# Optimization experiments

Hardware: AMD Instinct MI355X
Metric: run time of the kernel (lower is better)

Reference implementation:

```python
import jax, jax.numpy as jnp
import numpy as np

N_HEAD = 16


def setup_inputs() -> dict:
    key = jax.random.key(0)
    ks = jax.random.split(key, 4)
    B, S, NX = 2, 2048, 1024
    x = jax.random.normal(ks[0], (B, S, NX), dtype=jnp.float32)
    # additive causal mask: 0 where j <= i, -1e9 where j > i
    causal = jnp.tril(jnp.ones((S, S), dtype=jnp.float32))
    attention_mask = ((1.0 - causal) * -1e9)[None, None, :, :]
    w_attn = jax.random.normal(ks[1], (NX, 3 * NX), dtype=jnp.float32) * 0.02
    b_attn = jnp.zeros((3 * NX,), dtype=jnp.float32)
    w_proj = jax.random.normal(ks[2], (NX, NX), dtype=jnp.float32) * 0.02
    b_proj = jnp.zeros((NX,), dtype=jnp.float32)
    return {"x": x, "attention_mask": attention_mask, "w_attn": w_attn,
            "b_attn": b_attn, "w_proj": w_proj, "b_proj": b_proj}


def reference(x, attention_mask, w_attn, b_attn, w_proj, b_proj):
    B, S, NX = x.shape
    H = N_HEAD
    D = NX // H
    # c_attn (Conv1D): x @ W + b -> [B, S, 3*NX]
    qkv = jnp.einsum('bse,ef->bsf', x, w_attn) + b_attn
    q, k, v = jnp.split(qkv, 3, axis=-1)
    # split heads -> [B, H, S, D]
    q = q.reshape(B, S, H, D).transpose(0, 2, 1, 3)
    k = k.reshape(B, S, H, D).transpose(0, 2, 1, 3)
    v = v.reshape(B, S, H, D).transpose(0, 2, 1, 3)
    # scores [B, H, S, S], scaled by 1/sqrt(head_dim) since scale=True
    w = jnp.einsum('bhqd,bhkd->bhqk', q, k) / jnp.sqrt(jnp.float32(D))
    w = w + attention_mask
    w = jax.nn.softmax(w, axis=-1)
    # attn_dropout is identity in eval / p=0
    a = jnp.einsum('bhqk,bhkd->bhqd', w, v)
    # merge heads -> [B, S, NX]
    a = a.transpose(0, 2, 1, 3).reshape(B, S, NX)
    # c_proj (Conv1D)
    out = jnp.einsum('bse,ef->bsf', a, w_proj) + b_proj
    # resid_dropout identity
    return out
```

## Files before the change

### kernel.cpp

```cpp
#include <hip/hip_runtime.h>
#include <hip/hip_bf16.h>

typedef __bf16 bf16;
typedef __bf16 bf16x8 __attribute__((ext_vector_type(8)));
typedef __bf16 bf16x4 __attribute__((ext_vector_type(4)));
typedef float  f32x4  __attribute__((ext_vector_type(4)));
typedef float  f32x16 __attribute__((ext_vector_type(16)));

#define MFMA16(A,B,C) __builtin_amdgcn_mfma_f32_16x16x32_bf16(A,B,C,0,0,0)
#define MFMA32(A,B,C) __builtin_amdgcn_mfma_f32_32x32x16_bf16(A,B,C,0,0,0)
#define EXP2(x) __builtin_amdgcn_exp2f(x)

static constexpr int SEQ = 2048;
static constexpr int NXC = 1024;
#define QSCALE 0.1803368801111244f

static __device__ inline unsigned packb(float lo, float hi) {
  union { bf16 h[2]; unsigned u; } x;
  x.h[0] = (bf16)lo; x.h[1] = (bf16)hi;
  return x.u;
}
static __device__ inline bf16x8 frag_from_words(unsigned a, unsigned b,
                                                unsigned c, unsigned d) {
  union { unsigned u[4]; bf16x8 v; } x;
  x.u[0] = a; x.u[1] = b; x.u[2] = c; x.u[3] = d;
  return x.v;
}
__device__ __forceinline__ void gload16(const bf16* g, bf16* l) {
  __builtin_amdgcn_global_load_lds(
      (const __attribute__((address_space(1))) void*)g,
      (__attribute__((address_space(3))) void*)l, 16, 0, 0);
}

__global__ __launch_bounds__(256) void f2b_kernel(const float* __restrict__ in,
                                                  bf16* __restrict__ out, int n4) {
  int i = blockIdx.x * blockDim.x + threadIdx.x;
  if (i < n4) {
    float4 v = ((const float4*)in)[i];
    bf16x4 o;
    o[0] = (bf16)v.x; o[1] = (bf16)v.y; o[2] = (bf16)v.z; o[3] = (bf16)v.w;
    ((bf16x4*)out)[i] = o;
  }
}

__global__ __launch_bounds__(256) void tr_f2b(const float* __restrict__ in,
                                              bf16* __restrict__ out, int R, int C) {
  __shared__ bf16 t[64][72];
  const int c0 = blockIdx.x * 64, r0 = blockIdx.y * 64;
  const int tid = threadIdx.x;
  const int lr = tid >> 4, lc = (tid & 15) * 4;
  #pragma unroll
  for (int p = 0; p < 4; ++p) {
    int rr = lr + p * 16;
    float4 v = *(const float4*)&in[(size_t)(r0 + rr) * C + c0 + lc];
    t[lc + 0][rr] = (bf16)v.x; t[lc + 1][rr] = (bf16)v.y;
    t[lc + 2][rr] = (bf16)v.z; t[lc + 3][rr] = (bf16)v.w;
  }
  __syncthreads();
  const int orow = tid >> 3, ocol = (tid & 7) * 8;
  #pragma unroll
  for (int p = 0; p < 2; ++p) {
    int rr = orow + p * 32;
    *(bf16x8*)&out[(size_t)(c0 + rr) * R + r0 + ocol] = *(const bf16x8*)&t[rr][ocol];
  }
}

template<int MODE>
__global__ __launch_bounds__(256, 3) void gemm_bt(
    const bf16* __restrict__ A, const bf16* __restrict__ BT,
    const float* __restrict__ bias,
    bf16* __restrict__ qb, bf16* __restrict__ kb, bf16* __restrict__ vtb,
    float* __restrict__ outf, int K, int N, int nb)
{
  __shared__ bf16 As[2][128 * 32];
  __shared__ bf16 Bs[2][128 * 32];

  const int tid  = threadIdx.x;
  const int lane = tid & 63;
  const int w    = tid >> 6;
  const int cpx  = gridDim.x >> 3;
  const int swzb = (blockIdx.x & 7) * cpx + (blockIdx.x >> 3);
  const int m0   = (swzb / nb) * 128;
  const int n0   = (swzb % nb) * 128;
  const int wrow = (w >> 1) * 64;
  const int wcol = (w & 1) * 64;
  const int g    = lane >> 4;
  const int c16  = lane & 15;

  f32x4 acc[4][4];
  #pragma unroll
  for (int i = 0; i < 4; ++i)
    #pragma unroll
    for (int j = 0; j < 4; ++j)
      acc[i][j] = f32x4{0.f, 0.f, 0.f, 0.f};

  const int srow = lane >> 2;
  const int scol = ((lane & 3) ^ ((lane >> 3) & 3)) * 8;
  const bf16* gA = A  + (size_t)(m0 + w * 16 + srow) * K + scol;
  const bf16* gB = BT + (size_t)(n0 + w * 16 + srow) * K + scol;
  const size_t rstep = (size_t)64 * K;
  const int rchunk = (g ^ ((c16 >> 1) & 3)) * 8;

  const int NT = K >> 5;

  auto STAGE = [&](int b, int k0) {
    bf16* lA = &As[b][w * 512];
    bf16* lB = &Bs[b][w * 512];
    gload16(gA + k0,         lA);
    gload16(gA + k0 + rstep, lA + 64 * 32);
    gload16(gB + k0,         lB);
    gload16(gB + k0 + rstep, lB + 64 * 32);
  };

  STAGE(0, 0);
  __syncthreads();

  int cur = 0;
  for (int t = 0; t < NT; ++t) {
    if (t + 1 < NT) STAGE(cur ^ 1, (t + 1) << 5);

    const bf16* pa = &As[cur][0];
    const bf16* pb = &Bs[cur][0];
    bf16x8 af[4], bfr[4];
    #pragma unroll
    for (int i = 0; i < 4; ++i)
      af[i] = *(const bf16x8*)&pa[(wrow + i * 16 + c16) * 32 + rchunk];
    #pragma unroll
    for (int j = 0; j < 4; ++j)
      bfr[j] = *(const bf16x8*)&pb[(wcol + j * 16 + c16) * 32 + rchunk];
    #pragma unroll
    for (int i = 0; i < 4; ++i)
      #pragma unroll
      for (int j = 0; j < 4; ++j)
        acc[i][j] = MFMA16(af[i], bfr[j], acc[i][j]);

    __syncthreads();
    cur ^= 1;
  }

  #pragma unroll
  for (int i = 0; i < 4; ++i) {
    #pragma unroll
    for (int j = 0; j < 4; ++j) {
      #pragma unroll
      for (int r = 0; r < 4; ++r) {
        int gm = m0 + wrow + i * 16 + g * 4 + r;
        int gn = n0 + wcol + j * 16 + c16;
        float v = acc[i][j][r] + bias[gn];
        if (MODE == 0) {
          int which = gn >> 10;
          int cc = gn & 1023;
          int hh = cc >> 6, dd = cc & 63;
          int bb = gm >> 11, ss = gm & 2047;
          int bh = bb * 16 + hh;
          if (which == 0)
            qb[((size_t)bh * SEQ + ss) * 64 + dd] = (bf16)(v * QSCALE);
          else if (which == 1)
            kb[((size_t)bh * SEQ + ss) * 64 + dd] = (bf16)v;
          else
            vtb[((size_t)bh * 64 + dd) * SEQ + ss] = (bf16)v;
        } else {
          outf[(size_t)gm * N + gn] = v;
        }
      }
    }
  }
}

__global__ __launch_bounds__(256, 2) void attn9_kernel(
    const bf16* __restrict__ q, const bf16* __restrict__ k,
    const bf16* __restrict__ vt, bf16* __restrict__ aout)
{
  __shared__ bf16 smem[2][8192];

  const int tid  = threadIdx.x;
  const int lane = tid & 63;
  const int w    = tid >> 6;
  const int hi   = lane >> 5;
  const int q_l  = lane & 31;
  const int bid  = blockIdx.x;
  const int bh   = bid & 31;
  const int idx8 = (bid & 255) >> 5;
  const int strip= (bid >> 8) ? idx8 : 15 - idx8;
  const int qr0  = strip * 128 + w * 32;
  const int qg   = qr0 + q_l;
  const int nt   = 2 * strip + 2;

  bf16x8 qf[4];
  {
    const bf16* qp = q + ((size_t)bh * SEQ + qr0 + q_l) * 64 + hi * 8;
    #pragma unroll
    for (int c = 0; c < 4; ++c) qf[c] = *(const bf16x8*)(qp + c * 16);
  }

  f32x16 Ot0 = (f32x16)0.f, Ot1 = (f32x16)0.f;
  float mrun = -INFINITY, lrun = 0.f;

  const int r1 = tid >> 3;
  const int c1 = (tid & 7) ^ (r1 & 7);
  const bf16* kB = k  + (size_t)bh * SEQ * 64;
  const bf16* vB = vt + (size_t)bh * 64 * SEQ;
  const int sw = q_l & 7;

  auto STAGE = [&](int b, int kv0) {
    bf16* buf = &smem[b][0];
    gload16(kB + (size_t)(kv0 + r1) * 64 + c1 * 8,       buf + w * 512);
    gload16(kB + (size_t)(kv0 + r1 + 32) * 64 + c1 * 8,  buf + 2048 + w * 512);
    gload16(vB + (size_t)r1 * SEQ + kv0 + c1 * 8,        buf + 4096 + w * 512);
    gload16(vB + (size_t)(r1 + 32) * SEQ + kv0 + c1 * 8, buf + 6144 + w * 512);
  };

  auto do_tile = [&](int b, int kv0) {
    const bf16* Kb = &smem[b][0];
    const bf16* Vb = &smem[b][4096];

    bf16x8 kf[8];
    #pragma unroll
    for (int c = 0; c < 4; ++c) {
      int ch = ((2 * c + hi) ^ sw) * 8;
      kf[c]     = *(const bf16x8*)&Kb[q_l * 64 + ch];
      kf[4 + c] = *(const bf16x8*)&Kb[(q_l + 32) * 64 + ch];
    }

    f32x16 st0 = (f32x16)0.f, st1 = (f32x16)0.f;
    __builtin_amdgcn_s_setprio(1);
    #pragma unroll
    for (int c = 0; c < 4; ++c) {
      st0 = MFMA32(kf[c],     qf[c], st0);
      st1 = MFMA32(kf[4 + c], qf[c], st1);
    }
    __builtin_amdgcn_s_setprio(0);

    bf16x8 vf[8];
    #pragma unroll
    for (int t2 = 0; t2 < 2; ++t2)
      #pragma unroll
      for (int h = 0; h < 2; ++h) {
        int ch = ((4 * t2 + 2 * h + hi) ^ sw) * 8;
        vf[t2 * 2 + h]     = *(const bf16x8*)&Vb[q_l * 64 + ch];
        vf[4 + t2 * 2 + h] = *(const bf16x8*)&Vb[(q_l + 32) * 64 + ch];
      }

    if (kv0 + 63 > qr0) {
      #pragma unroll
      for (int r = 0; r < 16; ++r) {
        int kvl = kv0 + (r & 3) + 8 * (r >> 2) + 4 * hi;
        if (kvl > qg)      st0[r] = -1e30f;
        if (kvl + 32 > qg) st1[r] = -1e30f;
      }
    }

    float m8[8];
    #pragma unroll
    for (int r = 0; r < 8; ++r)
      m8[r] = fmaxf(fmaxf(st0[r], st0[r + 8]), fmaxf(st1[r], st1[r + 8]));
    #pragma unroll
    for (int r = 0; r < 4; ++r) m8[r] = fmaxf(m8[r], m8[r + 4]);
    float pmax = fmaxf(fmaxf(m8[0], m8[1]), fmaxf(m8[2], m8[3]));

    float mnew;
    if (__all(pmax <= mrun + 8.f)) {
      mnew = mrun;
    } else {
      float pm = fmaxf(pmax, __shfl_xor(pmax, 32));
      mnew = fmaxf(mrun, pm);
      const float sc = EXP2(mrun - mnew);
      lrun *= sc;
      Ot0 *= sc;
      Ot1 *= sc;
      mrun = mnew;
    }

    #pragma unroll
    for (int r = 0; r < 16; ++r) {
      st0[r] = EXP2(st0[r] - mnew);
      st1[r] = EXP2(st1[r] - mnew);
    }

    float s8[8];
    #pragma unroll
    for (int r = 0; r < 8; ++r)
      s8[r] = (st0[r] + st0[r + 8]) + (st1[r] + st1[r + 8]);
    #pragma unroll
    for (int r = 0; r < 4; ++r) s8[r] += s8[r + 4];
    lrun += (s8[0] + s8[1]) + (s8[2] + s8[3]);

    unsigned pw[16];
    #pragma unroll
    for (int m = 0; m < 8; ++m) {
      pw[m]     = packb(st0[2 * m], st0[2 * m + 1]);
      pw[8 + m] = packb(st1[2 * m], st1[2 * m + 1]);
    }
    __builtin_amdgcn_s_setprio(1);
    #pragma unroll
    for (int t2 = 0; t2 < 2; ++t2) {
      #pragma unroll
      for (int h = 0; h < 2; ++h) {
        auto sa = __builtin_amdgcn_permlane32_swap((int)pw[t2 * 8 + 4 * h + 0],
                                                   (int)pw[t2 * 8 + 4 * h + 2], false, false);
        auto sb = __builtin_amdgcn_permlane32_swap((int)pw[t2 * 8 + 4 * h + 1],
                                                   (int)pw[t2 * 8 + 4 * h + 3], false, false);
        bf16x8 pb = frag_from_words((unsigned)sa[0], (unsigned)sb[0],
                                    (unsigned)sa[1], (unsigned)sb[1]);
        Ot0 = MFMA32(vf[t2 * 2 + h],     pb, Ot0);
        Ot1 = MFMA32(vf[4 + t2 * 2 + h], pb, Ot1);
      }
    }
    __builtin_amdgcn_s_setprio(0);
  };

  STAGE(0, 0);
  asm volatile("s_waitcnt vmcnt(0)" ::: "memory");
  __builtin_amdgcn_s_barrier();

  int cur = 0;
  for (int t = 0; t < nt - 1; ++t) {
    STAGE(cur ^ 1, (t + 1) << 6);
    if ((t << 6) <= qr0 + 31) do_tile(cur, t << 6);
    asm volatile("s_waitcnt vmcnt(0)" ::: "memory");
    __builtin_amdgcn_s_barrier();
    cur ^= 1;
  }
  do_tile(cur, (nt - 1) << 6);

  lrun += __shfl_xor(lrun, 32);
  const float inv = 1.f / lrun;

  __syncthreads();
  bf16* ot = &smem[0][0];
  const int orow = w * 32 + q_l;
  #pragma unroll
  for (int r = 0; r < 16; ++r) {
    int d = (r & 3) + 8 * (r >> 2) + 4 * hi;
    ot[orow * 72 + d]      = (bf16)(Ot0[r] * inv);
    ot[orow * 72 + d + 32] = (bf16)(Ot1[r] * inv);
  }
  __syncthreads();

  const int bb = bh >> 4, hh = bh & 15;
  const int qrow = w * 32 + (lane >> 1), half = lane & 1;
  const bf16* src = ot + qrow * 72 + half * 32;
  bf16* dst = aout + ((size_t)bb * SEQ + strip * 128 + qrow) * NXC + hh * 64 + half * 32;
  #pragma unroll
  for (int e = 0; e < 4; ++e)
    *(bf16x8*)(dst + e * 8) = *(const bf16x8*)(src + e * 8);
}

extern "C" void kernel_launch(void* const* d_in, const int* in_sizes, int n_in,
                              void* d_out, int out_size, void* d_ws, size_t ws_size,
                              hipStream_t stream) {
  const float* x      = (const float*)d_in[0];
  const float* w_attn = (const float*)d_in[2];
  const float* b_attn = (const float*)d_in[3];
  const float* w_proj = (const float*)d_in[4];
  const float* b_proj = (const float*)d_in[5];
  float* out = (float*)d_out;

  char* p = (char*)d_ws;
  bf16* xb   = (bf16*)p; p += (size_t)4194304 * 2;
  bf16* wabT = (bf16*)p; p += (size_t)3145728 * 2;
  bf16* wpbT = (bf16*)p; p += (size_t)1048576 * 2;
  bf16* qb   = (bf16*)p; p += (size_t)4194304 * 2;
  bf16* kb   = (bf16*)p; p += (size_t)4194304 * 2;
  bf16* vtb  = (bf16*)p; p += (size_t)4194304 * 2;
  bf16* ab   = (bf16*)p; p += (size_t)4194304 * 2;

  f2b_kernel<<<4096, 256, 0, stream>>>(x, xb, 1048576);
  tr_f2b<<<dim3(48, 16), 256, 0, stream>>>(w_attn, wabT, 1024, 3072);
  tr_f2b<<<dim3(16, 16), 256, 0, stream>>>(w_proj, wpbT, 1024, 1024);

  gemm_bt<0><<<768, 256, 0, stream>>>(xb, wabT, b_attn, qb, kb, vtb,
                                      nullptr, 1024, 3072, 24);
  attn9_kernel<<<512, 256, 0, stream>>>(qb, kb, vtb, ab);
  gemm_bt<1><<<256, 256, 0, stream>>>(ab, wpbT, b_proj, nullptr, nullptr,
                                      nullptr, out, 1024, 1024, 8);
}
```

Baseline: 117.2 us.

## Merge prep kernels into one launch and stage attention KV tiles in pairs

Folds the three conversion and transpose launches into a single prep_kernel that dispatches on block index. This removes two kernel launches. The attention kernel now uses four LDS buffers and stages two 64-key tiles per iteration, which halves the number of barrier and wait points per strip. In exchange, static LDS per block doubles to 64KB, which could reduce occupancy below the two blocks per CU requested by the launch bounds.

Result: faster. 112.2 us (-4.2%).

```diff
diff --git a/kernel.cpp b/kernel.cpp
--- a/kernel.cpp
+++ b/kernel.cpp
@@ -32,22 +32,33 @@
       (__attribute__((address_space(3))) void*)l, 16, 0, 0);
 }
 
-__global__ __launch_bounds__(256) void f2b_kernel(const float* __restrict__ in,
-                                                  bf16* __restrict__ out, int n4) {
-  int i = blockIdx.x * blockDim.x + threadIdx.x;
-  if (i < n4) {
-    float4 v = ((const float4*)in)[i];
+__global__ __launch_bounds__(256) void prep_kernel(
+    const float* __restrict__ x, const float* __restrict__ w_attn,
+    const float* __restrict__ w_proj,
+    bf16* __restrict__ xb, bf16* __restrict__ wabT, bf16* __restrict__ wpbT)
+{
+  __shared__ bf16 t[64][72];
+  const int bid = blockIdx.x;
+  const int tid = threadIdx.x;
+
+  if (bid < 4096) {
+    int i = bid * 256 + tid;
+    float4 v = ((const float4*)x)[i];
     bf16x4 o;
     o[0] = (bf16)v.x; o[1] = (bf16)v.y; o[2] = (bf16)v.z; o[3] = (bf16)v.w;
-    ((bf16x4*)out)[i] = o;
-  }
-}
-
-__global__ __launch_bounds__(256) void tr_f2b(const float* __restrict__ in,
-                                              bf16* __restrict__ out, int R, int C) {
-  __shared__ bf16 t[64][72];
-  const int c0 = blockIdx.x * 64, r0 = blockIdx.y * 64;
-  const int tid = threadIdx.x;
+    ((bf16x4*)xb)[i] = o;
+    return;
+  }
+
+  const float* in;
+  bf16* out;
+  int R, C, l;
+  if (bid < 4864) { in = w_attn; out = wabT; R = 1024; C = 3072; l = bid - 4096;
+                    }
+  else            { in = w_proj; out = wpbT; R = 1024; C = 1024; l = bid - 4864; }
+  const int nbx = C >> 6;
+  const int c0 = (l % nbx) * 64, r0 = (l / nbx) * 64;
+
   const int lr = tid >> 4, lc = (tid & 15) * 4;
   #pragma unroll
   for (int p = 0; p < 4; ++p) {
@@ -167,11 +178,11 @@
   }
 }
 
-__global__ __launch_bounds__(256, 2) void attn9_kernel(
+__global__ __launch_bounds__(256, 2) void attn10_kernel(
     const bf16* __restrict__ q, const bf16* __restrict__ k,
     const bf16* __restrict__ vt, bf16* __restrict__ aout)
 {
-  __shared__ bf16 smem[2][8192];
+  __shared__ bf16 smem[4][8192];
 
   const int tid  = threadIdx.x;
   const int lane = tid & 63;
@@ -185,6 +196,7 @@
   const int qr0  = strip * 128 + w * 32;
   const int qg   = qr0 + q_l;
   const int nt   = 2 * strip + 2;
+  const int nst2 = nt >> 1;
 
   bf16x8 qf[4];
   {
@@ -310,18 +322,22 @@
   };
 
   STAGE(0, 0);
+  STAGE(1, 64);
   asm volatile("s_waitcnt vmcnt(0)" ::: "memory");
   __builtin_amdgcn_s_barrier();
 
-  int cur = 0;
-  for (int t = 0; t < nt - 1; ++t) {
-    STAGE(cur ^ 1, (t + 1) << 6);
-    if ((t << 6) <= qr0 + 31) do_tile(cur, t << 6);
+  int pair = 0;
+  for (int s = 0; s < nst2; ++s) {
+    if (s + 1 < nst2) {
+      STAGE(pair ^ 2,       (2 * s + 2) << 6);
+      STAGE((pair ^ 2) + 1, (2 * s + 3) << 6);
+    }
+    if (((2 * s) << 6) <= qr0 + 31)     do_tile(pair,     (2 * s) << 6);
+    if (((2 * s + 1) << 6) <= qr0 + 31) do_tile(pair + 1, (2 * s + 1) << 6);
     asm volatile("s_waitcnt vmcnt(0)" ::: "memory");
     __builtin_amdgcn_s_barrier();
-    cur ^= 1;
-  }
-  do_tile(cur, (nt - 1) << 6);
+    pair ^= 2;
+  }
 
   lrun += __shfl_xor(lrun, 32);
   const float inv = 1.f / lrun;
@@ -365,13 +381,11 @@
   bf16* vtb  = (bf16*)p; p += (size_t)4194304 * 2;
   bf16* ab   = (bf16*)p; p += (size_t)4194304 * 2;
 
-  f2b_kernel<<<4096, 256, 0, stream>>>(x, xb, 1048576);
-  tr_f2b<<<dim3(48, 16), 256, 0, stream>>>(w_attn, wabT, 1024, 3072);
-  tr_f2b<<<dim3(16, 16), 256, 0, stream>>>(w_proj, wpbT, 1024, 1024);
+  prep_kernel<<<5120, 256, 0, stream>>>(x, w_attn, w_proj, xb, wabT, wpbT);
 
   gemm_bt<0><<<768, 256, 0, stream>>>(xb, wabT, b_attn, qb, kb, vtb,
                                       nullptr, 1024, 3072, 24);
-  attn9_kernel<<<512, 256, 0, stream>>>(qb, kb, vtb, ab);
+  attn10_kernel<<<512, 256, 0, stream>>>(qb, kb, vtb, ab);
   gemm_bt<1><<<256, 256, 0, stream>>>(ab, wpbT, b_proj, nullptr, nullptr,
                                       nullptr, out, 1024, 1024, 8);
 }
```
